# Kernel optimization log

Hardware: AMD Instinct MI355X
Metric: run time of the kernel (lower is better)

## Reference

```python
import jax, jax.numpy as jnp
import numpy as np

H = 128      # hidden_units
L = 200      # maxlen
B = 2048     # batch of sequences
E = 8        # num_experts
SW = 64      # switch hidden dim


def setup_inputs() -> dict:
    key = jax.random.key(0)
    ks = jax.random.split(key, 16)
    s = 0.05
    inp = {
        "x": jax.random.normal(ks[0], (B, L, H), jnp.float32),
        "x_real": jax.random.normal(ks[1], (1, L, H), jnp.float32),
        "user_embedding": jax.random.normal(ks[2], (1, H), jnp.float32),
        # uexpert: conv1d(H,H,1) -> relu -> conv1d(H,H,1); weights [out,in]
        "uW1": jax.random.normal(ks[3], (H, H), jnp.float32) * s,
        "ub1": jax.random.normal(ks[4], (H,), jnp.float32) * s,
        "uW2": jax.random.normal(ks[5], (H, H), jnp.float32) * s,
        "ub2": jax.random.normal(ks[6], (H,), jnp.float32) * s,
        # stacked expert weights [E, out, in]
        "eW1": jax.random.normal(ks[7], (E, H, H), jnp.float32) * s,
        "eb1": jax.random.normal(ks[8], (E, H), jnp.float32) * s,
        "eW2": jax.random.normal(ks[9], (E, H, H), jnp.float32) * s,
        "eb2": jax.random.normal(ks[10], (E, H), jnp.float32) * s,
        # switch MLP: H -> SW -> E
        "sW1": jax.random.normal(ks[11], (SW, H), jnp.float32) * s,
        "sb1": jax.random.normal(ks[12], (SW,), jnp.float32) * s,
        "sW2": jax.random.normal(ks[13], (E, SW), jnp.float32) * s,
        "sb2": jax.random.normal(ks[14], (E,), jnp.float32) * s,
    }
    return inp


def _ffn(x, W1, b1, W2, b2):
    # conv1d(k=1) -> (dropout: identity at eval) -> relu -> conv1d(k=1) -> dropout
    h = jax.nn.relu(jnp.einsum("blh,oh->blo", x, W1) + b1)
    return jnp.einsum("blh,oh->blo", h, W2) + b2


def reference(x, x_real, user_embedding, uW1, ub1, uW2, ub2,
              eW1, eb1, eW2, eb2, sW1, sb1, sW2, sb2):
    # client_rep == 'avg': mean over the sequence of x_real -> [H]
    x_input = jnp.mean(x_real[0], axis=0)
    # switch MLP with ReLU on all but last layer
    h = jax.nn.relu(x_input @ sW1.T + sb1)
    logits = h @ sW2.T + sb2                      # [E]
    route_prob = jax.nn.softmax(logits, axis=-1)
    route = jnp.argmax(route_prob, axis=-1)       # scalar expert index
    out_prob_max = route_prob[route]
    # selected expert branch
    expert_out = _ffn(x, eW1[route], eb1[route], eW2[route], eb2[route])
    # always-on uexpert branch
    uexpert_out = _ffn(x, uW1, ub1, uW2, ub2)
    final_output = expert_out + uexpert_out       # [B, L, H]
    return (final_output, route, out_prob_max)
```

## Files before the change

kernel.cpp:

```cpp
#include <hip/hip_runtime.h>

#define HD 128
#define LSEQ 200
#define BATCH 2048
#define NE 8
#define SWH 64

#define BM 32
#define LDX 136
#define LDH 264
#define LDO 132
#define NTILES ((BATCH * LSEQ) / BM)
#define GRID 512

typedef float f32x4 __attribute__((ext_vector_type(4)));
typedef __bf16 bf16x4 __attribute__((ext_vector_type(4)));
typedef __bf16 bf16x8 __attribute__((ext_vector_type(8)));

#define BAR() do {                                          \
    asm volatile("s_waitcnt lgkmcnt(0)" ::: "memory");      \
    __builtin_amdgcn_sched_barrier(0);                      \
    __builtin_amdgcn_s_barrier();                           \
    __builtin_amdgcn_sched_barrier(0);                      \
} while (0)

static __device__ __forceinline__ unsigned short f2bf(float f) {
    union { float f; unsigned u; } v; v.f = f;
    unsigned u = v.u;
    u += 0x7fffu + ((u >> 16) & 1u);
    return (unsigned short)(u >> 16);
}

__global__ void prep_route(const float* __restrict__ x_real,
                           const float* __restrict__ sW1, const float* __restrict__ sb1,
                           const float* __restrict__ sW2, const float* __restrict__ sb2,
                           const float* __restrict__ uW1, const float* __restrict__ ub1,
                           const float* __restrict__ uW2, const float* __restrict__ ub2,
                           const float* __restrict__ eW1, const float* __restrict__ eb1,
                           const float* __restrict__ eW2, const float* __restrict__ eb2,
                           float* __restrict__ out_tail,
                           unsigned short* __restrict__ W1c, unsigned short* __restrict__ W2c,
                           float* __restrict__ b1c, float* __restrict__ b2s) {
    __shared__ float part[256];
    __shared__ float xm[HD];
    __shared__ float hsw[SWH];
    __shared__ float logits[NE];
    __shared__ int route_s;
    const int t = threadIdx.x;

    {
        int col = t & 127, half = t >> 7;
        float s = 0.f;
        for (int l = half * 100; l < half * 100 + 100; ++l) s += x_real[l * HD + col];
        part[t] = s;
    }
    __syncthreads();
    if (t < HD) xm[t] = (part[t] + part[t + 128]) * (1.0f / LSEQ);
    __syncthreads();
    if (t < SWH) {
        float s = sb1[t];
        for (int k = 0; k < HD; ++k) s += xm[k] * sW1[t * HD + k];
        hsw[t] = s > 0.f ? s : 0.f;
    }
    __syncthreads();
    if (t < NE) {
        float s = sb2[t];
        for (int k = 0; k < SWH; ++k) s += hsw[k] * sW2[t * SWH + k];
        logits[t] = s;
    }
    __syncthreads();
    if (t == 0) {
        float mx = logits[0]; int am = 0;
        for (int e = 1; e < NE; ++e) if (logits[e] > mx) { mx = logits[e]; am = e; }
        float den = 0.f;
        for (int e = 0; e < NE; ++e) den += __expf(logits[e] - mx);
        route_s = am;
        if (blockIdx.x == 0) {
            out_tail[0] = (float)am;
            out_tail[1] = 1.0f / den;
        }
    }
    __syncthreads();
    const int r = route_s;

    const int i = blockIdx.x * 256 + t;
    if (i < 2 * HD * HD) {
        int o = i >> 7, k = i & 127;
        float v1 = (o < HD) ? uW1[o * HD + k] : eW1[r * HD * HD + (o - HD) * HD + k];
        W1c[i] = f2bf(v1);
        int o2 = i >> 8, j = i & 255;
        float v2 = (j < HD) ? uW2[o2 * HD + j] : eW2[r * HD * HD + o2 * HD + (j - HD)];
        W2c[i] = f2bf(v2);
    }
    if (i < 2 * HD) b1c[i] = (i < HD) ? ub1[i] : eb1[r * HD + (i - HD)];
    if (i < HD)     b2s[i] = ub2[i] + eb2[r * HD + i];
}

__global__ __launch_bounds__(512, 4)
void moe_main(const float* __restrict__ x,
              const unsigned short* __restrict__ W1c, const unsigned short* __restrict__ W2c,
              const float* __restrict__ b1c, const float* __restrict__ b2s,
              float* __restrict__ out) {
    __shared__ __align__(16) unsigned short xs[BM * LDX];
    __shared__ __align__(16) unsigned short hs[BM * LDH];
    __shared__ __align__(16) float os[BM * LDO];

    const int t = threadIdx.x;
    const int lane = t & 63;
    const int w = t >> 6;
    const int l16 = lane & 15;
    const int lq = lane >> 4;
    const int ncb = w * 32;
    const int ncb2 = w * 16;

    bf16x8 w1[4][2];
    bf16x8 w2[8];
#pragma unroll
    for (int ks = 0; ks < 4; ++ks)
#pragma unroll
        for (int ht = 0; ht < 2; ++ht)
            w1[ks][ht] = *(const bf16x8*)&W1c[(ncb + ht * 16 + l16) * HD + ks * 32 + lq * 8];
#pragma unroll
    for (int ks = 0; ks < 8; ++ks)
        w2[ks] = *(const bf16x8*)&W2c[(ncb2 + l16) * 256 + ks * 32 + lq * 8];

    f32x4 bias1v[2], bias2v;
#pragma unroll
    for (int ht = 0; ht < 2; ++ht) bias1v[ht] = *(const f32x4*)&b1c[ncb + ht * 16 + lq * 4];
    bias2v = *(const f32x4*)&b2s[ncb2 + lq * 4];

    const int srow0 = t >> 5;
    const int sc4 = (t & 31) * 4;
    const int orow = t >> 5;
    const int ocol = (t & 31) * 4;

    int tile = blockIdx.x;
    float4 pv[2];
    {
        const float4* x4 = (const float4*)(x + (size_t)tile * (BM * HD));
#pragma unroll
        for (int i = 0; i < 2; ++i) pv[i] = x4[t + i * 512];
    }

    while (tile < NTILES) {
        const int ntile = tile + GRID;

#pragma unroll
        for (int i = 0; i < 2; ++i) {
            bf16x4 b;
            b[0] = (__bf16)pv[i].x; b[1] = (__bf16)pv[i].y;
            b[2] = (__bf16)pv[i].z; b[3] = (__bf16)pv[i].w;
            *(bf16x4*)&xs[(srow0 + i * 16) * LDX + sc4] = b;
        }

        if (ntile < NTILES) {
            const float4* x4 = (const float4*)(x + (size_t)ntile * (BM * HD));
#pragma unroll
            for (int i = 0; i < 2; ++i) pv[i] = x4[t + i * 512];
        }
        BAR();

        f32x4 acc1[2][2] = {};
#pragma unroll
        for (int ks = 0; ks < 4; ++ks) {
            const int kofs = ks * 32 + lq * 8;
            bf16x8 xf[2];
#pragma unroll
            for (int tt = 0; tt < 2; ++tt)
                xf[tt] = *(const bf16x8*)&xs[(tt * 16 + l16) * LDX + kofs];
#pragma unroll
            for (int ht = 0; ht < 2; ++ht)
#pragma unroll
                for (int tt = 0; tt < 2; ++tt)
                    acc1[ht][tt] = __builtin_amdgcn_mfma_f32_16x16x32_bf16(
                        w1[ks][ht], xf[tt], acc1[ht][tt], 0, 0, 0);
        }
#pragma unroll
        for (int ht = 0; ht < 2; ++ht)
#pragma unroll
            for (int tt = 0; tt < 2; ++tt) {
                bf16x4 hv;
#pragma unroll
                for (int r = 0; r < 4; ++r) {
                    float v = acc1[ht][tt][r] + bias1v[ht][r];
                    hv[r] = (__bf16)(v > 0.f ? v : 0.f);
                }
                *(bf16x4*)&hs[(tt * 16 + l16) * LDH + ncb + ht * 16 + lq * 4] = hv;
            }
        BAR();

#pragma unroll
        for (int tt = 0; tt < 2; ++tt) {
            f32x4 acc2 = {};
#pragma unroll
            for (int ks = 0; ks < 8; ++ks) {
                bf16x8 hf = *(const bf16x8*)&hs[(tt * 16 + l16) * LDH + ks * 32 + lq * 8];
                acc2 = __builtin_amdgcn_mfma_f32_16x16x32_bf16(w2[ks], hf, acc2, 0, 0, 0);
            }
            f32x4 o;
#pragma unroll
            for (int r = 0; r < 4; ++r) o[r] = acc2[r] + bias2v[r];
            *(f32x4*)&os[(tt * 16 + l16) * LDO + ncb2 + lq * 4] = o;
        }
        BAR();

        {
            float* outp = out + (size_t)tile * (BM * HD);
            f32x4 a = *(const f32x4*)&os[orow * LDO + ocol];
            f32x4 b = *(const f32x4*)&os[(16 + orow) * LDO + ocol];
            __builtin_nontemporal_store(a, (f32x4*)(outp + t * 4));
            __builtin_nontemporal_store(b, (f32x4*)(outp + 2048 + t * 4));
        }

        tile = ntile;
    }
}

extern "C" void kernel_launch(void* const* d_in, const int* in_sizes, int n_in,
                              void* d_out, int out_size, void* d_ws, size_t ws_size,
                              hipStream_t stream) {
    const float* x      = (const float*)d_in[0];
    const float* x_real = (const float*)d_in[1];
    const float* uW1 = (const float*)d_in[3];
    const float* ub1 = (const float*)d_in[4];
    const float* uW2 = (const float*)d_in[5];
    const float* ub2 = (const float*)d_in[6];
    const float* eW1 = (const float*)d_in[7];
    const float* eb1 = (const float*)d_in[8];
    const float* eW2 = (const float*)d_in[9];
    const float* eb2 = (const float*)d_in[10];
    const float* sW1 = (const float*)d_in[11];
    const float* sb1 = (const float*)d_in[12];
    const float* sW2 = (const float*)d_in[13];
    const float* sb2 = (const float*)d_in[14];
    float* out = (float*)d_out;

    char* ws = (char*)d_ws;
    unsigned short* W1c = (unsigned short*)(ws + 64);
    unsigned short* W2c = (unsigned short*)(ws + 64 + 65536);
    float* b1c = (float*)(ws + 64 + 131072);
    float* b2s = (float*)(ws + 64 + 131072 + 1024);

    prep_route<<<128, 256, 0, stream>>>(x_real, sW1, sb1, sW2, sb2,
                                        uW1, ub1, uW2, ub2, eW1, eb1, eW2, eb2,
                                        out + (size_t)BATCH * LSEQ * HD,
                                        W1c, W2c, b1c, b2s);
    moe_main<<<GRID, 512, 0, stream>>>(x, W1c, W2c, b1c, b2s, out);
}
```

Measured before the change: 82.10 us.

## Double-buffer x tile in LDS and software-pipeline output stores to drop a barrier

Restructures the persistent tile loop into a fixed-count software pipeline. The x staging buffer is double-buffered, the next tile's LDS write overlaps the current GEMM1, and the previous tile's output store moves to the start of the next iteration. This cuts the barriers per tile from three to two and adds overlap between global loads, stores and MFMA work. It relies on NTILES being exactly KITER*GRID and uses more LDS, which may lower occupancy.

```diff
diff --git a/kernel.cpp b/kernel.cpp
--- a/kernel.cpp
+++ b/kernel.cpp
@@ -12,6 +12,7 @@
 #define LDO 132
 #define NTILES ((BATCH * LSEQ) / BM)
 #define GRID 512
+#define KITER 25
 
 typedef float f32x4 __attribute__((ext_vector_type(4)));
 typedef __bf16 bf16x4 __attribute__((ext_vector_type(4)));
@@ -101,7 +102,7 @@
               const unsigned short* __restrict__ W1c, const unsigned short* __restrict__ W2c,
               const float* __restrict__ b1c, const float* __restrict__ b2s,
               float* __restrict__ out) {
-    __shared__ __align__(16) unsigned short xs[BM * LDX];
+    __shared__ __align__(16) unsigned short xs[2][BM * LDX];
     __shared__ __align__(16) unsigned short hs[BM * LDH];
     __shared__ __align__(16) float os[BM * LDO];
 
@@ -134,61 +135,80 @@
     const int orow = t >> 5;
     const int ocol = (t & 31) * 4;
 
-    int tile = blockIdx.x;
+    const int t0 = blockIdx.x;
     float4 pv[2];
+
     {
-        const float4* x4 = (const float4*)(x + (size_t)tile * (BM * HD));
-#pragma unroll
-        for (int i = 0; i < 2; ++i) pv[i] = x4[t + i * 512];
-    }
-
-    while (tile < NTILES) {
-        const int ntile = tile + GRID;
-
+        const float4* x4 = (const float4*)(x + (size_t)t0 * (BM * HD));
+        pv[0] = x4[t]; pv[1] = x4[t + 512];
 #pragma unroll
         for (int i = 0; i < 2; ++i) {
             bf16x4 b;
             b[0] = (__bf16)pv[i].x; b[1] = (__bf16)pv[i].y;
             b[2] = (__bf16)pv[i].z; b[3] = (__bf16)pv[i].w;
-            *(bf16x4*)&xs[(srow0 + i * 16) * LDX + sc4] = b;
-        }
-
-        if (ntile < NTILES) {
-            const float4* x4 = (const float4*)(x + (size_t)ntile * (BM * HD));
-#pragma unroll
-            for (int i = 0; i < 2; ++i) pv[i] = x4[t + i * 512];
+            *(bf16x4*)&xs[0][(srow0 + i * 16) * LDX + sc4] = b;
+        }
+        const float4* x4b = (const float4*)(x + (size_t)(t0 + GRID) * (BM * HD));
+        pv[0] = x4b[t]; pv[1] = x4b[t + 512];
+    }
+    BAR();
+
+    for (int i = 0; i < KITER; ++i) {
+        const int tile = t0 + i * GRID;
+        const unsigned short* xsr = xs[i & 1];
+        unsigned short* xsw = xs[(i + 1) & 1];
+
+        if (i >= 1) {
+            float* outp = out + (size_t)(tile - GRID) * (BM * HD);
+            f32x4 a = *(const f32x4*)&os[orow * LDO + ocol];
+            f32x4 b = *(const f32x4*)&os[(16 + orow) * LDO + ocol];
+            __builtin_nontemporal_store(a, (f32x4*)(outp + t * 4));
+            __builtin_nontemporal_store(b, (f32x4*)(outp + 2048 + t * 4));
+        }
+        if (i <= KITER - 2) {
+#pragma unroll
+            for (int j = 0; j < 2; ++j) {
+                bf16x4 b;
+                b[0] = (__bf16)pv[j].x; b[1] = (__bf16)pv[j].y;
+                b[2] = (__bf16)pv[j].z; b[3] = (__bf16)pv[j].w;
+                *(bf16x4*)&xsw[(srow0 + j * 16) * LDX + sc4] = b;
+            }
+        }
+        {
+            f32x4 acc1[2][2] = {};
+#pragma unroll
+            for (int ks = 0; ks < 4; ++ks) {
+                const int kofs = ks * 32 + lq * 8;
+                bf16x8 xf[2];
+#pragma unroll
+                for (int tt = 0; tt < 2; ++tt)
+                    xf[tt] = *(const bf16x8*)&xsr[(tt * 16 + l16) * LDX + kofs];
+#pragma unroll
+                for (int ht = 0; ht < 2; ++ht)
+#pragma unroll
+                    for (int tt = 0; tt < 2; ++tt)
+                        acc1[ht][tt] = __builtin_amdgcn_mfma_f32_16x16x32_bf16(
+                            w1[ks][ht], xf[tt], acc1[ht][tt], 0, 0, 0);
+            }
+#pragma unroll
+            for (int ht = 0; ht < 2; ++ht)
+#pragma unroll
+                for (int tt = 0; tt < 2; ++tt) {
+                    bf16x4 hv;
+#pragma unroll
+                    for (int r = 0; r < 4; ++r) {
+                        float v = acc1[ht][tt][r] + bias1v[ht][r];
+                        hv[r] = (__bf16)(v > 0.f ? v : 0.f);
+                    }
+                    *(bf16x4*)&hs[(tt * 16 + l16) * LDH + ncb + ht * 16 + lq * 4] = hv;
+                }
         }
         BAR();
 
-        f32x4 acc1[2][2] = {};
-#pragma unroll
-        for (int ks = 0; ks < 4; ++ks) {
-            const int kofs = ks * 32 + lq * 8;
-            bf16x8 xf[2];
-#pragma unroll
-            for (int tt = 0; tt < 2; ++tt)
-                xf[tt] = *(const bf16x8*)&xs[(tt * 16 + l16) * LDX + kofs];
-#pragma unroll
-            for (int ht = 0; ht < 2; ++ht)
-#pragma unroll
-                for (int tt = 0; tt < 2; ++tt)
-                    acc1[ht][tt] = __builtin_amdgcn_mfma_f32_16x16x32_bf16(
-                        w1[ks][ht], xf[tt], acc1[ht][tt], 0, 0, 0);
-        }
-#pragma unroll
-        for (int ht = 0; ht < 2; ++ht)
-#pragma unroll
-            for (int tt = 0; tt < 2; ++tt) {
-                bf16x4 hv;
-#pragma unroll
-                for (int r = 0; r < 4; ++r) {
-                    float v = acc1[ht][tt][r] + bias1v[ht][r];
-                    hv[r] = (__bf16)(v > 0.f ? v : 0.f);
-                }
-                *(bf16x4*)&hs[(tt * 16 + l16) * LDH + ncb + ht * 16 + lq * 4] = hv;
-            }
-        BAR();
-
+        if (i <= KITER - 3) {
+            const float4* x4n = (const float4*)(x + (size_t)(tile + 2 * GRID) * (BM * HD));
+            pv[0] = x4n[t]; pv[1] = x4n[t + 512];
+        }
 #pragma unroll
         for (int tt = 0; tt < 2; ++tt) {
             f32x4 acc2 = {};
@@ -203,16 +223,14 @@
             *(f32x4*)&os[(tt * 16 + l16) * LDO + ncb2 + lq * 4] = o;
         }
         BAR();
-
-        {
-            float* outp = out + (size_t)tile * (BM * HD);
-            f32x4 a = *(const f32x4*)&os[orow * LDO + ocol];
-            f32x4 b = *(const f32x4*)&os[(16 + orow) * LDO + ocol];
-            __builtin_nontemporal_store(a, (f32x4*)(outp + t * 4));
-            __builtin_nontemporal_store(b, (f32x4*)(outp + 2048 + t * 4));
-        }
-
-        tile = ntile;
+    }
+
+    {
+        float* outp = out + (size_t)(t0 + (KITER - 1) * GRID) * (BM * HD);
+        f32x4 a = *(const f32x4*)&os[orow * LDO + ocol];
+        f32x4 b = *(const f32x4*)&os[(16 + orow) * LDO + ocol];
+        __builtin_nontemporal_store(a, (f32x4*)(outp + t * 4));
+        __builtin_nontemporal_store(b, (f32x4*)(outp + 2048 + t * 4));
     }
 }
 
```

Measured after the change: 81.22 us. Within noise of the previous version (-1.1%).
